# Optimization experiments

Hardware: AMD Instinct MI355X
Metric: run time of the kernel (lower is better)

Reference implementation:

```python
import jax, jax.numpy as jnp
import numpy as np

B, D, H, W, C = 2, 28, 28, 28, 96
HEADS = 3
WS = (7, 7, 7)
SS = (3, 3, 3)
N = WS[0] * WS[1] * WS[2]  # 343 tokens per window
MLP_DIM = 4 * C


def _rel_pos_index():
    coords = np.stack(np.meshgrid(np.arange(WS[0]), np.arange(WS[1]), np.arange(WS[2]), indexing='ij'))
    cf = coords.reshape(3, -1)
    rel = (cf[:, :, None] - cf[:, None, :]).transpose(1, 2, 0)
    rel[..., 0] += WS[0] - 1
    rel[..., 1] += WS[1] - 1
    rel[..., 2] += WS[2] - 1
    rel[..., 0] *= (2 * WS[1] - 1) * (2 * WS[2] - 1)
    rel[..., 1] *= 2 * WS[2] - 1
    return rel.sum(-1)  # [N, N] int


def _compute_mask():
    # shifted-window attention mask (MONAI compute_mask)
    img = np.zeros((1, D, H, W, 1), np.float32)
    cnt = 0.0
    for ds in (slice(0, -WS[0]), slice(-WS[0], -SS[0]), slice(-SS[0], None)):
        for hs in (slice(0, -WS[1]), slice(-WS[1], -SS[1]), slice(-SS[1], None)):
            for ws_ in (slice(0, -WS[2]), slice(-WS[2], -SS[2]), slice(-SS[2], None)):
                img[:, ds, hs, ws_, :] = cnt
                cnt += 1.0
    mw = img.reshape(1, D // WS[0], WS[0], H // WS[1], WS[1], W // WS[2], WS[2], 1)
    mw = mw.transpose(0, 1, 3, 5, 2, 4, 6, 7).reshape(-1, N)  # [nw, N]
    diff = mw[:, None, :] - mw[:, :, None]
    return np.where(diff != 0, -100.0, 0.0).astype(np.float32)  # [nw, N, N]


def _ln(x, g, b):
    mu = x.mean(-1, keepdims=True)
    var = ((x - mu) ** 2).mean(-1, keepdims=True)
    return (x - mu) * jax.lax.rsqrt(var + 1e-5) * g + b


def setup_inputs() -> dict:
    key = jax.random.key(0)
    ks = jax.random.split(key, 8)
    f = lambda k, shape: (jax.random.normal(k, shape) * 0.02).astype(jnp.float32)
    n_bias = (2 * WS[0] - 1) * (2 * WS[1] - 1) * (2 * WS[2] - 1)
    return {
        'x': jax.random.normal(ks[0], (B, D, H, W, C), jnp.float32),
        'mask_matrix': jnp.asarray(_compute_mask()),
        'g1': jnp.ones((C,), jnp.float32), 'b1': jnp.zeros((C,), jnp.float32),
        'w_qkv': f(ks[1], (3 * C, C)), 'b_qkv': jnp.zeros((3 * C,), jnp.float32),
        'bias_table': f(ks[2], (n_bias, HEADS)),
        'w_proj': f(ks[3], (C, C)), 'b_proj': jnp.zeros((C,), jnp.float32),
        'g2': jnp.ones((C,), jnp.float32), 'b2': jnp.zeros((C,), jnp.float32),
        'w_fc1': f(ks[4], (MLP_DIM, C)), 'b_fc1': jnp.zeros((MLP_DIM,), jnp.float32),
        'w_fc2': f(ks[5], (C, MLP_DIM)), 'b_fc2': jnp.zeros((C,), jnp.float32),
        'rel_index': jnp.asarray(_rel_pos_index(), dtype=jnp.int32),
    }


def reference(x, mask_matrix, g1, b1, w_qkv, b_qkv, bias_table, w_proj, b_proj,
              g2, b2, w_fc1, b_fc1, w_fc2, b_fc2, rel_index):
    shortcut = x
    h = _ln(x, g1, b1)
    # cyclic shift
    h = jnp.roll(h, (-SS[0], -SS[1], -SS[2]), axis=(1, 2, 3))
    # window partition -> [B_, N, C]
    win = h.reshape(B, D // WS[0], WS[0], H // WS[1], WS[1], W // WS[2], WS[2], C)
    win = win.transpose(0, 1, 3, 5, 2, 4, 6, 7).reshape(-1, N, C)
    Bw = win.shape[0]
    hd = C // HEADS
    qkv = (win @ w_qkv.T + b_qkv).reshape(Bw, N, 3, HEADS, hd).transpose(2, 0, 3, 1, 4)
    q, k, v = qkv[0] * (hd ** -0.5), qkv[1], qkv[2]
    attn = jnp.einsum('bhnd,bhmd->bhnm', q, k)  # [Bw, H, N, N]
    bias = bias_table[rel_index.reshape(-1)].reshape(N, N, HEADS).transpose(2, 0, 1)
    attn = attn + bias[None]
    nw = mask_matrix.shape[0]
    attn = attn.reshape(Bw // nw, nw, HEADS, N, N) + mask_matrix[None, :, None]
    attn = jax.nn.softmax(attn.reshape(Bw, HEADS, N, N), axis=-1)
    out = jnp.einsum('bhnm,bhmd->bhnd', attn, v).transpose(0, 2, 1, 3).reshape(Bw, N, C)
    out = out @ w_proj.T + b_proj
    # window reverse -> [B, D, H, W, C]
    out = out.reshape(B, D // WS[0], H // WS[1], W // WS[2], WS[0], WS[1], WS[2], C)
    out = out.transpose(0, 1, 4, 2, 5, 3, 6, 7).reshape(B, D, H, W, C)
    # reverse cyclic shift
    out = jnp.roll(out, SS, axis=(1, 2, 3))
    x = shortcut + out
    h2 = _ln(x, g2, b2)
    h2 = jax.nn.gelu(h2 @ w_fc1.T + b_fc1, approximate=False)
    return x + (h2 @ w_fc2.T + b_fc2)
```

## Files before the change

### kernel.cpp

```cpp
#include <hip/hip_runtime.h>
#include <hip/hip_bf16.h>
#include <math.h>

typedef unsigned short u16;
typedef unsigned int u32;
typedef unsigned char u8;

#define T_TOK 43904
#define NTOK 343
#define LOG2E 1.4426950408889634f
#define MASKV 144.26950408889634f

typedef __attribute__((ext_vector_type(4))) float f32x4;
typedef __attribute__((ext_vector_type(8))) short s16x8;

__device__ __forceinline__ float bf2f(u32 v) { return __uint_as_float(v << 16); }
__device__ __forceinline__ u16 f2bf(float f) {
  u32 u = __float_as_uint(f);
  return (u16)((u + 0x7fffu + ((u >> 16) & 1u)) >> 16);
}

__device__ __forceinline__ float ldf(const void* p, int f32, size_t i) {
  return f32 ? ((const float*)p)[i] : bf2f(((const u16*)p)[i]);
}
__device__ __forceinline__ float2 ld2(const void* p, int f32, size_t i) {
  if (f32) return *(const float2*)((const float*)p + i);
  u32 pk = *(const u32*)((const u16*)p + i);
  return make_float2(bf2f(pk & 0xffff), bf2f(pk >> 16));
}

__device__ __forceinline__ size_t spatial_base(int t) {
  int win = t / 343, n = t - win * 343;
  int bb = win >> 6, wrem = win & 63;
  int wd = wrem >> 4, wh = (wrem >> 2) & 3, ww = wrem & 3;
  int td = n / 49; int r = n - td * 49; int th = r / 7; int tw = r - th * 7;
  int d0 = wd * 7 + td + 3; if (d0 >= 28) d0 -= 28;
  int h0 = wh * 7 + th + 3; if (h0 >= 28) h0 -= 28;
  int w0 = ww * 7 + tw + 3; if (w0 >= 28) w0 -= 28;
  return (size_t)(((bb * 28 + d0) * 28 + h0) * 28 + w0) * 96;
}

__device__ __forceinline__ int zone3(int p) { return p < 21 ? 0 : (p < 25 ? 1 : 2); }
__device__ __forceinline__ int cid_of(int mw, int n) {
  int td = n / 49, rr = n - td * 49, th = rr / 7, tw = rr - th * 7;
  int d = (mw >> 4) * 7 + td, h = ((mw >> 2) & 3) * 7 + th, w = (mw & 3) * 7 + tw;
  return zone3(d) * 9 + zone3(h) * 3 + zone3(w);
}

__global__ __launch_bounds__(64) void detect_kernel(const u16* __restrict__ x, int* __restrict__ flag) {
  int lane = threadIdx.x;
  int bad = 0;
  #pragma unroll
  for (int q = 0; q < 8; q++) {
    u16 b = x[(lane * 8 + q) * 2];
    int e = (b >> 7) & 0xff;
    if (e >= 0x90) bad = 1;
  }
  unsigned long long m = __ballot(bad);
  if (lane == 0) *flag = (m != 0ull) ? 1 : 0;
}

__global__ __launch_bounds__(256) void wconv_kernel(
    const void* __restrict__ w0, const void* __restrict__ w1,
    const void* __restrict__ w2, const void* __restrict__ w3,
    u16* __restrict__ out, const int* __restrict__ dflag) {
  int f32 = __builtin_amdgcn_readfirstlane(dflag[0]);
  int g = blockIdx.x * 256 + threadIdx.x;
  if (g >= 110592) return;
  float v;
  if (g < 27648)      v = ldf(w0, f32, g);
  else if (g < 36864) v = ldf(w1, f32, g - 27648);
  else if (g < 73728) v = ldf(w2, f32, g - 36864);
  else                v = ldf(w3, f32, g - 73728);
  out[g] = f2bf(v);
}

__global__ __launch_bounds__(256) void ln_gather_kernel(
    const void* __restrict__ x, const void* __restrict__ g, const void* __restrict__ b,
    u16* __restrict__ outw, const int* __restrict__ dflag) {
  int f32 = __builtin_amdgcn_readfirstlane(dflag[0]);
  int t = blockIdx.x * 4 + (threadIdx.x >> 6);
  int lane = threadIdx.x & 63;
  size_t base = spatial_base(t);
  int c = lane * 2;
  float vx = 0.f, vy = 0.f;
  if (c < 96) { float2 p = ld2(x, f32, base + c); vx = p.x; vy = p.y; }
  float s = vx + vy, ss = vx * vx + vy * vy;
  #pragma unroll
  for (int o = 1; o < 64; o <<= 1) { s += __shfl_xor(s, o); ss += __shfl_xor(ss, o); }
  float mean = s * (1.f / 96.f);
  float var = ss * (1.f / 96.f) - mean * mean;
  float rstd = rsqrtf(var + 1e-5f);
  if (c < 96) {
    float2 gp = ld2(g, f32, c), bp = ld2(b, f32, c);
    float y0 = (vx - mean) * rstd * gp.x + bp.x;
    float y1 = (vy - mean) * rstd * gp.y + bp.y;
    *(u32*)(outw + (size_t)t * 96 + c) = (u32)f2bf(y0) | ((u32)f2bf(y1) << 16);
  }
}

__global__ __launch_bounds__(256) void b3m_kernel(
    const void* __restrict__ bias_table, const int* __restrict__ rel,
    u16* __restrict__ b3m, const int* __restrict__ dflag) {
  int f32 = __builtin_amdgcn_readfirstlane(dflag[0]);
  int row = blockIdx.x;
  int by = blockIdx.y;
  int cls = by / 3, head = by - cls * 3;
  int mw = ((cls & 4) ? 48 : 0) | ((cls & 2) ? 12 : 0) | ((cls & 1) ? 3 : 0);
  int cidq = cid_of(mw, row);
  for (int col = threadIdx.x; col < 352; col += 256) {
    float v = -MASKV;
    if (col < 343) {
      v = ldf(bias_table, f32, (size_t)rel[row * 343 + col] * 3 + head) * LOG2E;
      if (cid_of(mw, col) != cidq) v -= MASKV;
    }
    b3m[((size_t)by * 343 + row) * 352 + col] = f2bf(v);
  }
}

__global__ __launch_bounds__(256) void qkv_kernel(
    const u16* __restrict__ A, const u16* __restrict__ Wb, const void* __restrict__ bias,
    u16* __restrict__ outp, const int* __restrict__ dflag) {
  int f32 = __builtin_amdgcn_readfirstlane(dflag[0]);
  __shared__ alignas(16) u16 As[128 * 104];
  __shared__ alignas(16) u16 Ws[96 * 104];
  int tid = threadIdx.x;
  int m0 = blockIdx.x * 128, n0 = blockIdx.y * 96;
  int w = tid >> 6, lane = tid & 63, quad = lane >> 4, l16 = lane & 15;
  f32x4 acc[2][6];
  #pragma unroll
  for (int i = 0; i < 2; i++)
    #pragma unroll
    for (int j = 0; j < 6; j++) acc[i][j] = (f32x4){0.f, 0.f, 0.f, 0.f};
  for (int i = tid; i < 1536; i += 256) {
    int row = i / 12; int c = (i - row * 12) * 8;
    *(uint4*)&As[row * 104 + c] = *(const uint4*)(A + (size_t)(m0 + row) * 96 + c);
  }
  for (int i = tid; i < 1152; i += 256) {
    int row = i / 12; int c = (i - row * 12) * 8;
    *(uint4*)&Ws[row * 104 + c] = *(const uint4*)(Wb + (size_t)(n0 + row) * 96 + c);
  }
  __syncthreads();
  #pragma unroll
  for (int kc = 0; kc < 3; kc++) {
    s16x8 fa0 = *(const s16x8*)&As[(w * 32 + l16) * 104 + kc * 32 + quad * 8];
    s16x8 fa1 = *(const s16x8*)&As[(w * 32 + 16 + l16) * 104 + kc * 32 + quad * 8];
    #pragma unroll
    for (int j = 0; j < 6; j++) {
      s16x8 fb = *(const s16x8*)&Ws[(j * 16 + l16) * 104 + kc * 32 + quad * 8];
      acc[0][j] = __builtin_amdgcn_mfma_f32_16x16x32_bf16(fa0, fb, acc[0][j], 0, 0, 0);
      acc[1][j] = __builtin_amdgcn_mfma_f32_16x16x32_bf16(fa1, fb, acc[1][j], 0, 0, 0);
    }
  }
  #pragma unroll
  for (int i = 0; i < 2; i++) {
    #pragma unroll
    for (int r = 0; r < 4; r++) {
      int mm = m0 + w * 32 + i * 16 + quad * 4 + r;
      #pragma unroll
      for (int j = 0; j < 6; j++) {
        int nn = n0 + j * 16 + l16;
        float v = acc[i][j][r] + ldf(bias, f32, nn);
        int sel = nn / 96, hd = (nn - sel * 96) >> 5, cc = nn & 31;
        float scl = (sel == 0) ? 0.25504208f : 1.0f;
        outp[((size_t)(sel * 3 + hd) * T_TOK + mm) * 32 + cc] = f2bf(v * scl);
      }
    }
  }
}

__device__ __forceinline__ int vsw(int ch) { return ((ch >> 1) ^ (ch >> 3)) & 3; }

__global__ __launch_bounds__(512) void attn_mfma_kernel(
    const u16* __restrict__ qkv, const u16* __restrict__ b3m,
    u16* __restrict__ attnb) {
  __shared__ alignas(16) u16 Ks[352 * 32];
  __shared__ alignas(16) u16 Vt[32 * 352];
  __shared__ alignas(16) u16 Ps[8][512];

  int tid = threadIdx.x;
  int wh = blockIdx.y;
  int head = wh % 3;
  int win = wh / 3;
  int mw = win & 63;
  int cls = (((mw >> 4) == 3) ? 4 : 0) | ((((mw >> 2) & 3) == 3) ? 2 : 0) | (((mw & 3) == 3) ? 1 : 0);
  int m0 = blockIdx.x * 128;
  size_t wbase = (size_t)win * NTOK;

  const u16* qplane = qkv + ((size_t)head * T_TOK + wbase) * 32;
  const u16* kplane = qkv + ((size_t)(3 + head) * T_TOK + wbase) * 32;
  const u16* vplane = qkv + ((size_t)(6 + head) * T_TOK + wbase) * 32;

  for (int i = tid; i < 1408; i += 512) {
    int tok = i >> 2, cb = i & 3;
    uint4 kv = make_uint4(0, 0, 0, 0);
    if (tok < 343) kv = *(const uint4*)(kplane + (size_t)tok * 32 + cb * 8);
    *(uint4*)&Ks[tok * 32 + 8 * (cb ^ (tok & 3))] = kv;
  }
  for (int i = tid; i < 688; i += 512) {
    int p = i >> 2, cb = (i & 3) * 8;
    int t0 = 2 * p;
    uint4 v0 = *(const uint4*)(vplane + (size_t)t0 * 32 + cb);
    uint4 v1 = make_uint4(0, 0, 0, 0);
    if (t0 + 1 < 343) v1 = *(const uint4*)(vplane + (size_t)(t0 + 1) * 32 + cb);
    u32 a0[4] = {v0.x, v0.y, v0.z, v0.w};
    u32 a1[4] = {v1.x, v1.y, v1.z, v1.w};
    int blk = t0 >> 3, tin = (t0 & 7) >> 1;
    #pragma unroll
    for (int q = 0; q < 4; q++) {
      int ch0 = cb + 2 * q;
      u32 w0v = (a0[q] & 0xffffu) | ((a1[q] & 0xffffu) << 16);
      u32 w1v = (a0[q] >> 16) | (a1[q] & 0xffff0000u);
      ((u32*)Vt)[ch0 * 176 + 4 * (blk ^ vsw(ch0)) + tin] = w0v;
      ((u32*)Vt)[(ch0 + 1) * 176 + 4 * (blk ^ vsw(ch0 + 1)) + tin] = w1v;
    }
  }
  if (tid < 256) {
    int ch = tid >> 3, j = tid & 7;
    Vt[ch * 352 + 8 * (43 ^ vsw(ch)) + j] = 0;
  }
  __syncthreads();

  int w = tid >> 6, lane = tid & 63, quad = lane >> 4, l16 = lane & 15;
  int qbase = m0 + w * 16;
  int qrow_l = qbase + l16;
  int qc = qrow_l < NTOK ? qrow_l : NTOK - 1;
  s16x8 fq = *(const s16x8*)(qplane + (size_t)qc * 32 + quad * 8);
  const u16* bmrow = b3m + ((size_t)(cls * 3 + head) * 343 + qc) * 352;
  int swl = (l16 ^ (l16 >> 2)) & 3;
  int vsw0 = vsw(l16), vsw1 = vsw(16 + l16);

  float lsum = 0.f;
  f32x4 o0 = {0.f, 0.f, 0.f, 0.f}, o1 = {0.f, 0.f, 0.f, 0.f};
  const f32x4 zz = {0.f, 0.f, 0.f, 0.f};

  for (int t32 = 0; t32 < 11; t32++) {
    #pragma unroll
    for (int h = 0; h < 2; h++) {
      int kb = t32 * 32 + h * 16;
      int ktok = kb + l16;
      s16x8 fk = *(const s16x8*)&Ks[ktok * 32 + 8 * (quad ^ (ktok & 3))];
      f32x4 st = __builtin_amdgcn_mfma_f32_16x16x32_bf16(fk, fq, zz, 0, 0, 0);
      uint2 bm = *(const uint2*)(bmrow + kb + quad * 4);
      float p0 = exp2f(st[0] + bf2f(bm.x & 0xffff));
      float p1 = exp2f(st[1] + bf2f(bm.x >> 16));
      float p2 = exp2f(st[2] + bf2f(bm.y & 0xffff));
      float p3 = exp2f(st[3] + bf2f(bm.y >> 16));
      lsum += (p0 + p1) + (p2 + p3);
      u32 pa = (__float_as_uint(p0) >> 16) | (__float_as_uint(p1) & 0xffff0000u);
      u32 pb = (__float_as_uint(p2) >> 16) | (__float_as_uint(p3) & 0xffff0000u);
      int blkp = h * 2 + (quad >> 1);
      *(uint2*)&Ps[w][l16 * 32 + 8 * (blkp ^ swl) + (quad & 1) * 4] = make_uint2(pa, pb);
    }
    s16x8 fp  = *(const s16x8*)&Ps[w][l16 * 32 + 8 * (quad ^ swl)];
    s16x8 fv0 = *(const s16x8*)&Vt[l16 * 352 + 8 * ((t32 * 4 + quad) ^ vsw0)];
    s16x8 fv1 = *(const s16x8*)&Vt[(16 + l16) * 352 + 8 * ((t32 * 4 + quad) ^ vsw1)];
    o0 = __builtin_amdgcn_mfma_f32_16x16x32_bf16(fp, fv0, o0, 0, 0, 0);
    o1 = __builtin_amdgcn_mfma_f32_16x16x32_bf16(fp, fv1, o1, 0, 0, 0);
  }

  lsum += __shfl_xor(lsum, 16);
  lsum += __shfl_xor(lsum, 32);
  #pragma unroll
  for (int r = 0; r < 4; r++) {
    int qrow = qbase + quad * 4 + r;
    float ls = __shfl(lsum, quad * 4 + r);
    if (qrow < NTOK) {
      float rs = 1.0f / ls;
      size_t ob = (wbase + qrow) * 96 + head * 32;
      attnb[ob + l16] = f2bf(o0[r] * rs);
      attnb[ob + 16 + l16] = f2bf(o1[r] * rs);
    }
  }
}

__global__ __launch_bounds__(256) void mlp_fused_kernel(
    const u16* __restrict__ attnb, const u16* __restrict__ wcat,
    const void* __restrict__ x, const void* __restrict__ b_proj,
    const void* __restrict__ g2, const void* __restrict__ b2,
    const void* __restrict__ b_fc1, const void* __restrict__ b_fc2,
    void* __restrict__ outp, const int* __restrict__ dflag) {
  int f32 = __builtin_amdgcn_readfirstlane(dflag[0]);
  __shared__ alignas(16) u16 As[64 * 104];
  __shared__ alignas(16) u16 As2[64 * 104];
  __shared__ alignas(16) u16 Ws[96 * 104];
  const u16* w_projb = wcat + 27648;
  const u16* w_fc1b  = wcat + 36864;
  const u16* w_fc2b  = wcat + 73728;
  int tid = threadIdx.x, m0 = blockIdx.x * 64;
  int w = tid >> 6, lane = tid & 63, quad = lane >> 4, l16 = lane & 15;

  for (int i = tid; i < 768; i += 256) {
    int row = i / 12, c = (i - row * 12) * 8;
    *(uint4*)&As[row * 104 + c] = *(const uint4*)(attnb + (size_t)(m0 + row) * 96 + c);
  }
  for (int i = tid; i < 1152; i += 256) {
    int row = i / 12, c = (i - row * 12) * 8;
    *(uint4*)&Ws[row * 104 + c] = *(const uint4*)(w_projb + row * 96 + c);
  }
  __syncthreads();
  f32x4 accp[6];
  #pragma unroll
  for (int j = 0; j < 6; j++) accp[j] = (f32x4){0.f, 0.f, 0.f, 0.f};
  #pragma unroll
  for (int kc = 0; kc < 3; kc++) {
    s16x8 fa = *(const s16x8*)&As[(w * 16 + l16) * 104 + kc * 32 + quad * 8];
    #pragma unroll
    for (int j = 0; j < 6; j++) {
      s16x8 fb = *(const s16x8*)&Ws[(j * 16 + l16) * 104 + kc * 32 + quad * 8];
      accp[j] = __builtin_amdgcn_mfma_f32_16x16x32_bf16(fa, fb, accp[j], 0, 0, 0);
    }
  }
  __syncthreads();

  float bp[6], gv[6], b2v[6];
  #pragma unroll
  for (int j = 0; j < 6; j++) {
    int nn = j * 16 + l16;
    bp[j] = ldf(b_proj, f32, nn); gv[j] = ldf(g2, f32, nn); b2v[j] = ldf(b2, f32, nn);
  }
  float rv[4][6];
  size_t sb[4];
  #pragma unroll
  for (int r = 0; r < 4; r++) {
    int mm = m0 + w * 16 + quad * 4 + r;
    sb[r] = spatial_base(mm);
    float s = 0.f, ss = 0.f;
    #pragma unroll
    for (int j = 0; j < 6; j++) {
      float v = accp[j][r] + bp[j] + ldf(x, f32, sb[r] + j * 16 + l16);
      rv[r][j] = v; s += v; ss += v * v;
    }
    #pragma unroll
    for (int o = 1; o < 16; o <<= 1) { s += __shfl_xor(s, o); ss += __shfl_xor(ss, o); }
    float mean = s * (1.f / 96.f);
    float var = ss * (1.f / 96.f) - mean * mean;
    float rstd = rsqrtf(var + 1e-5f);
    #pragma unroll
    for (int j = 0; j < 6; j++)
      As[(w * 16 + quad * 4 + r) * 104 + j * 16 + l16] = f2bf((rv[r][j] - mean) * rstd * gv[j] + b2v[j]);
  }

  f32x4 acc2[6];
  #pragma unroll
  for (int j = 0; j < 6; j++) acc2[j] = (f32x4){0.f, 0.f, 0.f, 0.f};
  for (int c = 0; c < 4; c++) {
    __syncthreads();
    for (int i = tid; i < 1152; i += 256) {
      int row = i / 12, cc = (i - row * 12) * 8;
      *(uint4*)&Ws[row * 104 + cc] = *(const uint4*)(w_fc1b + (size_t)(96 * c + row) * 96 + cc);
    }
    __syncthreads();
    f32x4 a1[6];
    #pragma unroll
    for (int j = 0; j < 6; j++) a1[j] = (f32x4){0.f, 0.f, 0.f, 0.f};
    #pragma unroll
    for (int kc = 0; kc < 3; kc++) {
      s16x8 fa = *(const s16x8*)&As[(w * 16 + l16) * 104 + kc * 32 + quad * 8];
      #pragma unroll
      for (int j = 0; j < 6; j++) {
        s16x8 fb = *(const s16x8*)&Ws[(j * 16 + l16) * 104 + kc * 32 + quad * 8];
        a1[j] = __builtin_amdgcn_mfma_f32_16x16x32_bf16(fa, fb, a1[j], 0, 0, 0);
      }
    }
    #pragma unroll
    for (int j = 0; j < 6; j++) {
      float bf1 = ldf(b_fc1, f32, 96 * c + j * 16 + l16);
      #pragma unroll
      for (int r = 0; r < 4; r++) {
        float v = a1[j][r] + bf1;
        v = 0.5f * v * (1.0f + erff(v * 0.70710678118f));
        As2[(w * 16 + quad * 4 + r) * 104 + j * 16 + l16] = f2bf(v);
      }
    }
    __syncthreads();
    for (int i = tid; i < 1152; i += 256) {
      int row = i / 12, cc = (i - row * 12) * 8;
      *(uint4*)&Ws[row * 104 + cc] = *(const uint4*)(w_fc2b + (size_t)row * 384 + 96 * c + cc);
    }
    __syncthreads();
    #pragma unroll
    for (int kc = 0; kc < 3; kc++) {
      s16x8 fa2 = *(const s16x8*)&As2[(w * 16 + l16) * 104 + kc * 32 + quad * 8];
      #pragma unroll
      for (int j = 0; j < 6; j++) {
        s16x8 fb = *(const s16x8*)&Ws[(j * 16 + l16) * 104 + kc * 32 + quad * 8];
        acc2[j] = __builtin_amdgcn_mfma_f32_16x16x32_bf16(fa2, fb, acc2[j], 0, 0, 0);
      }
    }
  }
  float bf2v[6];
  #pragma unroll
  for (int j = 0; j < 6; j++) bf2v[j] = ldf(b_fc2, f32, j * 16 + l16);
  #pragma unroll
  for (int r = 0; r < 4; r++) {
    #pragma unroll
    for (int j = 0; j < 6; j++) {
      float v = acc2[j][r] + bf2v[j] + rv[r][j];
      if (f32) ((float*)outp)[sb[r] + j * 16 + l16] = v;
      else     ((u16*)outp)[sb[r] + j * 16 + l16] = f2bf(v);
    }
  }
}

extern "C" void kernel_launch(void* const* d_in, const int* in_sizes, int n_in,
                              void* d_out, int out_size, void* d_ws, size_t ws_size,
                              hipStream_t stream) {
  (void)in_sizes; (void)n_in; (void)out_size; (void)ws_size;
  const void* x       = d_in[0];
  const void* g1      = d_in[2];
  const void* b1      = d_in[3];
  const void* w_qkv   = d_in[4];
  const void* b_qkv   = d_in[5];
  const void* bias_tb = d_in[6];
  const void* w_proj  = d_in[7];
  const void* b_proj  = d_in[8];
  const void* g2      = d_in[9];
  const void* b2      = d_in[10];
  const void* w_fc1   = d_in[11];
  const void* b_fc1   = d_in[12];
  const void* w_fc2   = d_in[13];
  const void* b_fc2   = d_in[14];
  const int* rel_idx  = (const int*)d_in[15];

  char* ws = (char*)d_ws;
  int*  dflag = (int*)ws;
  u16*  winb  = (u16*)(ws + 256);
  u16*  qkvb  = (u16*)(ws + 8429824);
  u16*  attnb = (u16*)(ws + 33718528);
  u16*  b3mb  = (u16*)(ws + 42148096);
  u16*  wcat  = (u16*)(ws + 47943424);
  u16*  w_qkvb = wcat;

  detect_kernel<<<1, 64, 0, stream>>>((const u16*)x, dflag);
  wconv_kernel<<<432, 256, 0, stream>>>(w_qkv, w_proj, w_fc1, w_fc2, wcat, dflag);
  b3m_kernel<<<dim3(343, 24), 256, 0, stream>>>(bias_tb, rel_idx, b3mb, dflag);
  ln_gather_kernel<<<T_TOK / 4, 256, 0, stream>>>(x, g1, b1, winb, dflag);
  qkv_kernel<<<dim3(343, 3), 256, 0, stream>>>(winb, w_qkvb, b_qkv, qkvb, dflag);
  attn_mfma_kernel<<<dim3(3, 384), 512, 0, stream>>>(qkvb, b3mb, attnb);
  mlp_fused_kernel<<<686, 256, 0, stream>>>(attnb, wcat, x, b_proj, g2, b2,
                                            b_fc1, b_fc2, d_out, dflag);
}
```

Measured before the change: 228.1 us.

## Load GEMM operands directly from global memory instead of staging in LDS

```diff
diff --git a/kernel.cpp b/kernel.cpp
--- a/kernel.cpp
+++ b/kernel.cpp
@@ -122,8 +122,6 @@
     const u16* __restrict__ A, const u16* __restrict__ Wb, const void* __restrict__ bias,
     u16* __restrict__ outp, const int* __restrict__ dflag) {
   int f32 = __builtin_amdgcn_readfirstlane(dflag[0]);
-  __shared__ alignas(16) u16 As[128 * 104];
-  __shared__ alignas(16) u16 Ws[96 * 104];
   int tid = threadIdx.x;
   int m0 = blockIdx.x * 128, n0 = blockIdx.y * 96;
   int w = tid >> 6, lane = tid & 63, quad = lane >> 4, l16 = lane & 15;
@@ -132,22 +130,13 @@
   for (int i = 0; i < 2; i++)
     #pragma unroll
     for (int j = 0; j < 6; j++) acc[i][j] = (f32x4){0.f, 0.f, 0.f, 0.f};
-  for (int i = tid; i < 1536; i += 256) {
-    int row = i / 12; int c = (i - row * 12) * 8;
-    *(uint4*)&As[row * 104 + c] = *(const uint4*)(A + (size_t)(m0 + row) * 96 + c);
-  }
-  for (int i = tid; i < 1152; i += 256) {
-    int row = i / 12; int c = (i - row * 12) * 8;
-    *(uint4*)&Ws[row * 104 + c] = *(const uint4*)(Wb + (size_t)(n0 + row) * 96 + c);
-  }
-  __syncthreads();
   #pragma unroll
   for (int kc = 0; kc < 3; kc++) {
-    s16x8 fa0 = *(const s16x8*)&As[(w * 32 + l16) * 104 + kc * 32 + quad * 8];
-    s16x8 fa1 = *(const s16x8*)&As[(w * 32 + 16 + l16) * 104 + kc * 32 + quad * 8];
+    s16x8 fa0 = *(const s16x8*)(A + (size_t)(m0 + w * 32 + l16) * 96 + kc * 32 + quad * 8);
+    s16x8 fa1 = *(const s16x8*)(A + (size_t)(m0 + w * 32 + 16 + l16) * 96 + kc * 32 + quad * 8);
     #pragma unroll
     for (int j = 0; j < 6; j++) {
-      s16x8 fb = *(const s16x8*)&Ws[(j * 16 + l16) * 104 + kc * 32 + quad * 8];
+      s16x8 fb = *(const s16x8*)(Wb + (size_t)(n0 + j * 16 + l16) * 96 + kc * 32 + quad * 8);
       acc[0][j] = __builtin_amdgcn_mfma_f32_16x16x32_bf16(fa0, fb, acc[0][j], 0, 0, 0);
       acc[1][j] = __builtin_amdgcn_mfma_f32_16x16x32_bf16(fa1, fb, acc[1][j], 0, 0, 0);
     }
@@ -283,35 +272,25 @@
   int f32 = __builtin_amdgcn_readfirstlane(dflag[0]);
   __shared__ alignas(16) u16 As[64 * 104];
   __shared__ alignas(16) u16 As2[64 * 104];
-  __shared__ alignas(16) u16 Ws[96 * 104];
   const u16* w_projb = wcat + 27648;
   const u16* w_fc1b  = wcat + 36864;
   const u16* w_fc2b  = wcat + 73728;
   int tid = threadIdx.x, m0 = blockIdx.x * 64;
   int w = tid >> 6, lane = tid & 63, quad = lane >> 4, l16 = lane & 15;
-
-  for (int i = tid; i < 768; i += 256) {
-    int row = i / 12, c = (i - row * 12) * 8;
-    *(uint4*)&As[row * 104 + c] = *(const uint4*)(attnb + (size_t)(m0 + row) * 96 + c);
-  }
-  for (int i = tid; i < 1152; i += 256) {
-    int row = i / 12, c = (i - row * 12) * 8;
-    *(uint4*)&Ws[row * 104 + c] = *(const uint4*)(w_projb + row * 96 + c);
-  }
-  __syncthreads();
+  int row = m0 + w * 16;
+
   f32x4 accp[6];
   #pragma unroll
   for (int j = 0; j < 6; j++) accp[j] = (f32x4){0.f, 0.f, 0.f, 0.f};
   #pragma unroll
   for (int kc = 0; kc < 3; kc++) {
-    s16x8 fa = *(const s16x8*)&As[(w * 16 + l16) * 104 + kc * 32 + quad * 8];
+    s16x8 fa = *(const s16x8*)(attnb + (size_t)(row + l16) * 96 + kc * 32 + quad * 8);
     #pragma unroll
     for (int j = 0; j < 6; j++) {
-      s16x8 fb = *(const s16x8*)&Ws[(j * 16 + l16) * 104 + kc * 32 + quad * 8];
+      s16x8 fb = *(const s16x8*)(w_projb + (size_t)(j * 16 + l16) * 96 + kc * 32 + quad * 8);
       accp[j] = __builtin_amdgcn_mfma_f32_16x16x32_bf16(fa, fb, accp[j], 0, 0, 0);
     }
   }
-  __syncthreads();
 
   float bp[6], gv[6], b2v[6];
   #pragma unroll
@@ -344,13 +323,8 @@
   f32x4 acc2[6];
   #pragma unroll
   for (int j = 0; j < 6; j++) acc2[j] = (f32x4){0.f, 0.f, 0.f, 0.f};
+  #pragma unroll
   for (int c = 0; c < 4; c++) {
-    __syncthreads();
-    for (int i = tid; i < 1152; i += 256) {
-      int row = i / 12, cc = (i - row * 12) * 8;
-      *(uint4*)&Ws[row * 104 + cc] = *(const uint4*)(w_fc1b + (size_t)(96 * c + row) * 96 + cc);
-    }
-    __syncthreads();
     f32x4 a1[6];
     #pragma unroll
     for (int j = 0; j < 6; j++) a1[j] = (f32x4){0.f, 0.f, 0.f, 0.f};
@@ -359,7 +333,7 @@
       s16x8 fa = *(const s16x8*)&As[(w * 16 + l16) * 104 + kc * 32 + quad * 8];
       #pragma unroll
       for (int j = 0; j < 6; j++) {
-        s16x8 fb = *(const s16x8*)&Ws[(j * 16 + l16) * 104 + kc * 32 + quad * 8];
+        s16x8 fb = *(const s16x8*)(w_fc1b + (size_t)(96 * c + j * 16 + l16) * 96 + kc * 32 + quad * 8);
         a1[j] = __builtin_amdgcn_mfma_f32_16x16x32_bf16(fa, fb, a1[j], 0, 0, 0);
       }
     }
@@ -373,22 +347,17 @@
         As2[(w * 16 + quad * 4 + r) * 104 + j * 16 + l16] = f2bf(v);
       }
     }
-    __syncthreads();
-    for (int i = tid; i < 1152; i += 256) {
-      int row = i / 12, cc = (i - row * 12) * 8;
-      *(uint4*)&Ws[row * 104 + cc] = *(const uint4*)(w_fc2b + (size_t)row * 384 + 96 * c + cc);
-    }
-    __syncthreads();
     #pragma unroll
     for (int kc = 0; kc < 3; kc++) {
       s16x8 fa2 = *(const s16x8*)&As2[(w * 16 + l16) * 104 + kc * 32 + quad * 8];
       #pragma unroll
       for (int j = 0; j < 6; j++) {
-        s16x8 fb = *(const s16x8*)&Ws[(j * 16 + l16) * 104 + kc * 32 + quad * 8];
+        s16x8 fb = *(const s16x8*)(w_fc2b + (size_t)(j * 16 + l16) * 384 + 96 * c + kc * 32 + quad * 8);
         acc2[j] = __builtin_amdgcn_mfma_f32_16x16x32_bf16(fa2, fb, acc2[j], 0, 0, 0);
       }
     }
   }
+
   float bf2v[6];
   #pragma unroll
   for (int j = 0; j < 6; j++) bf2v[j] = ldf(b_fc2, f32, j * 16 + l16);
```

Result: slower. 245.0 us (+7.4%).

## Fuse LayerNorm window gather into QKV GEMM and use cheaper erf approximation

Applied to the files above, without the earlier changes.

```diff
diff --git a/kernel.cpp b/kernel.cpp
--- a/kernel.cpp
+++ b/kernel.cpp
@@ -18,6 +18,16 @@
 __device__ __forceinline__ u16 f2bf(float f) {
   u32 u = __float_as_uint(f);
   return (u16)((u + 0x7fffu + ((u >> 16) & 1u)) >> 16);
+}
+
+__device__ __forceinline__ float erf_cheap(float x) {
+  float ax = fabsf(x);
+  float t = 1.0f / (1.0f + 0.3275911f * ax);
+  float poly = t * (0.254829592f + t * (-0.284496736f + t * (1.421413741f +
+               t * (-1.453152027f + t * 1.061405429f))));
+  float e = exp2f(-ax * ax * LOG2E);
+  float y = 1.0f - poly * e;
+  return copysignf(y, x);
 }
 
 __device__ __forceinline__ float ldf(const void* p, int f32, size_t i) {
@@ -73,30 +83,6 @@
   else if (g < 73728) v = ldf(w2, f32, g - 36864);
   else                v = ldf(w3, f32, g - 73728);
   out[g] = f2bf(v);
-}
-
-__global__ __launch_bounds__(256) void ln_gather_kernel(
-    const void* __restrict__ x, const void* __restrict__ g, const void* __restrict__ b,
-    u16* __restrict__ outw, const int* __restrict__ dflag) {
-  int f32 = __builtin_amdgcn_readfirstlane(dflag[0]);
-  int t = blockIdx.x * 4 + (threadIdx.x >> 6);
-  int lane = threadIdx.x & 63;
-  size_t base = spatial_base(t);
-  int c = lane * 2;
-  float vx = 0.f, vy = 0.f;
-  if (c < 96) { float2 p = ld2(x, f32, base + c); vx = p.x; vy = p.y; }
-  float s = vx + vy, ss = vx * vx + vy * vy;
-  #pragma unroll
-  for (int o = 1; o < 64; o <<= 1) { s += __shfl_xor(s, o); ss += __shfl_xor(ss, o); }
-  float mean = s * (1.f / 96.f);
-  float var = ss * (1.f / 96.f) - mean * mean;
-  float rstd = rsqrtf(var + 1e-5f);
-  if (c < 96) {
-    float2 gp = ld2(g, f32, c), bp = ld2(b, f32, c);
-    float y0 = (vx - mean) * rstd * gp.x + bp.x;
-    float y1 = (vy - mean) * rstd * gp.y + bp.y;
-    *(u32*)(outw + (size_t)t * 96 + c) = (u32)f2bf(y0) | ((u32)f2bf(y1) << 16);
-  }
 }
 
 __global__ __launch_bounds__(256) void b3m_kernel(
@@ -119,7 +105,8 @@
 }
 
 __global__ __launch_bounds__(256) void qkv_kernel(
-    const u16* __restrict__ A, const u16* __restrict__ Wb, const void* __restrict__ bias,
+    const void* __restrict__ x, const void* __restrict__ g1, const void* __restrict__ b1,
+    const u16* __restrict__ Wb, const void* __restrict__ bias,
     u16* __restrict__ outp, const int* __restrict__ dflag) {
   int f32 = __builtin_amdgcn_readfirstlane(dflag[0]);
   __shared__ alignas(16) u16 As[128 * 104];
@@ -127,20 +114,41 @@
   int tid = threadIdx.x;
   int m0 = blockIdx.x * 128, n0 = blockIdx.y * 96;
   int w = tid >> 6, lane = tid & 63, quad = lane >> 4, l16 = lane & 15;
-  f32x4 acc[2][6];
-  #pragma unroll
-  for (int i = 0; i < 2; i++)
-    #pragma unroll
-    for (int j = 0; j < 6; j++) acc[i][j] = (f32x4){0.f, 0.f, 0.f, 0.f};
-  for (int i = tid; i < 1536; i += 256) {
-    int row = i / 12; int c = (i - row * 12) * 8;
-    *(uint4*)&As[row * 104 + c] = *(const uint4*)(A + (size_t)(m0 + row) * 96 + c);
+
+  {
+    int row = tid >> 1, half = tid & 1;
+    size_t base = spatial_base(m0 + row) + half * 48;
+    float s = 0.f, ss = 0.f;
+    #pragma unroll
+    for (int cc = 0; cc < 48; cc += 2) {
+      float2 p = ld2(x, f32, base + cc);
+      s += p.x + p.y; ss += p.x * p.x + p.y * p.y;
+    }
+    s += __shfl_xor(s, 1); ss += __shfl_xor(ss, 1);
+    float mean = s * (1.f / 96.f);
+    float var = ss * (1.f / 96.f) - mean * mean;
+    float rstd = rsqrtf(var + 1e-5f);
+    u16* dst = &As[row * 104 + half * 48];
+    #pragma unroll
+    for (int cc = 0; cc < 48; cc += 2) {
+      float2 p = ld2(x, f32, base + cc);
+      float2 gp = ld2(g1, f32, half * 48 + cc), bp = ld2(b1, f32, half * 48 + cc);
+      float y0 = (p.x - mean) * rstd * gp.x + bp.x;
+      float y1 = (p.y - mean) * rstd * gp.y + bp.y;
+      *(u32*)(dst + cc) = (u32)f2bf(y0) | ((u32)f2bf(y1) << 16);
+    }
   }
   for (int i = tid; i < 1152; i += 256) {
     int row = i / 12; int c = (i - row * 12) * 8;
     *(uint4*)&Ws[row * 104 + c] = *(const uint4*)(Wb + (size_t)(n0 + row) * 96 + c);
   }
   __syncthreads();
+
+  f32x4 acc[2][6];
+  #pragma unroll
+  for (int i = 0; i < 2; i++)
+    #pragma unroll
+    for (int j = 0; j < 6; j++) acc[i][j] = (f32x4){0.f, 0.f, 0.f, 0.f};
   #pragma unroll
   for (int kc = 0; kc < 3; kc++) {
     s16x8 fa0 = *(const s16x8*)&As[(w * 32 + l16) * 104 + kc * 32 + quad * 8];
@@ -369,7 +377,7 @@
       #pragma unroll
       for (int r = 0; r < 4; r++) {
         float v = a1[j][r] + bf1;
-        v = 0.5f * v * (1.0f + erff(v * 0.70710678118f));
+        v = 0.5f * v * (1.0f + erf_cheap(v * 0.70710678118f));
         As2[(w * 16 + quad * 4 + r) * 104 + j * 16 + l16] = f2bf(v);
       }
     }
@@ -425,7 +433,6 @@
 
   char* ws = (char*)d_ws;
   int*  dflag = (int*)ws;
-  u16*  winb  = (u16*)(ws + 256);
   u16*  qkvb  = (u16*)(ws + 8429824);
   u16*  attnb = (u16*)(ws + 33718528);
   u16*  b3mb  = (u16*)(ws + 42148096);
@@ -435,8 +442,7 @@
   detect_kernel<<<1, 64, 0, stream>>>((const u16*)x, dflag);
   wconv_kernel<<<432, 256, 0, stream>>>(w_qkv, w_proj, w_fc1, w_fc2, wcat, dflag);
   b3m_kernel<<<dim3(343, 24), 256, 0, stream>>>(bias_tb, rel_idx, b3mb, dflag);
-  ln_gather_kernel<<<T_TOK / 4, 256, 0, stream>>>(x, g1, b1, winb, dflag);
-  qkv_kernel<<<dim3(343, 3), 256, 0, stream>>>(winb, w_qkvb, b_qkv, qkvb, dflag);
+  qkv_kernel<<<dim3(343, 3), 256, 0, stream>>>(x, g1, b1, w_qkvb, b_qkv, qkvb, dflag);
   attn_mfma_kernel<<<dim3(3, 384), 512, 0, stream>>>(qkvb, b3mb, attnb);
   mlp_fused_kernel<<<686, 256, 0, stream>>>(attnb, wcat, x, b_proj, g2, b2,
                                             b_fc1, b_fc2, d_out, dflag);
```

New measurement: 262.9 us. 15.2% more time.
